# Kernel tuning notes

Hardware: AMD Instinct MI355X
Metric: run time of the kernel (lower is better)

The kernel has to match this reference:

```python
import jax, jax.numpy as jnp
import numpy as np
from jax.scipy.linalg import expm

B, T, N_IN, N_HID, N_OUT = 8192, 2048, 2, 10, 10


def setup_inputs() -> dict:
    key = jax.random.key(0)
    k0, k1, k2, k3, k4 = jax.random.split(key, 5)
    inputs = jax.random.normal(k0, (B, T, N_IN), dtype=jnp.float32)
    # skew-symmetric seed for the orthogonal recurrent kernel (expm parametrization)
    A = jax.random.normal(k1, (N_HID, N_HID), dtype=jnp.float32) * 0.1
    # input_kernel: nn.Linear(n_inputs, n_hidden, bias=False) -> weight [H, D_in]
    W_in = jax.random.normal(k2, (N_HID, N_IN), dtype=jnp.float32) / np.sqrt(N_IN)
    # modrelu bias, initialized uniform(-0.01, 0.01) as in exprnn
    b_mod = jax.random.uniform(k3, (N_HID,), jnp.float32, -0.01, 0.01)
    # final nn.Linear(n_hidden, n_outputs)
    lin_W = jax.random.normal(k4, (N_OUT, N_HID), dtype=jnp.float32) / np.sqrt(N_HID)
    lin_b = jnp.zeros((N_OUT,), jnp.float32)
    return {"inputs": inputs, "A": A, "W_in": W_in, "b_mod": b_mod,
            "lin_W": lin_W, "lin_b": lin_b}


def _modrelu(z, b):
    # modrelu(z) = sign(z) * relu(|z| + b)
    return jnp.sign(z) * jax.nn.relu(jnp.abs(z) + b)


def reference(inputs, A, W_in, b_mod, lin_W, lin_b):
    # Orthogonal recurrent matrix: Bmat = expm(skew(A)), skew from strict upper triangle
    A_tri = jnp.triu(A, k=1)
    Bmat = expm(A_tri - A_tri.T)  # [H, H], orthogonal
    # Precompute input projections for all timesteps: [B, T, H]
    x_proj = jnp.einsum('btd,hd->bth', inputs, W_in)
    h0 = jnp.zeros((inputs.shape[0], W_in.shape[0]), dtype=inputs.dtype)

    def step(h, x_t):
        h_new = _modrelu(x_t + h @ Bmat, b_mod)
        return h_new, None

    hT, _ = jax.lax.scan(step, h0, jnp.swapaxes(x_proj, 0, 1))  # scan over time
    out = hT @ lin_W.T + lin_b  # [B, n_outputs]
    return out
```

## Files before the change

kernel.cpp:

```cpp
#include <hip/hip_runtime.h>
#include <hip/hip_bf16.h>

#define H 10
#define T_LEN 2048
#define BATCH 8192

__global__ void expm_kernel(const float* __restrict__ A, float* __restrict__ Bout) {
    __shared__ double S[H][H];
    __shared__ double P[H][H];
    __shared__ double E[H][H];
    const int tid = threadIdx.x;
    const int i = tid / H, j = tid % H;
    if (tid < H * H) {
        double a = 0.0;
        if (i < j) a = (double)A[i * H + j];
        else if (i > j) a = -(double)A[j * H + i];
        a *= (1.0 / 256.0);
        S[i][j] = a;
        P[i][j] = a;
        E[i][j] = (i == j ? 1.0 : 0.0) + a;
    }
    __syncthreads();
    for (int k = 2; k <= 16; ++k) {
        double acc = 0.0;
        if (tid < H * H) {
            for (int m = 0; m < H; ++m) acc += P[i][m] * S[m][j];
            acc *= (1.0 / (double)k);
        }
        __syncthreads();
        if (tid < H * H) { P[i][j] = acc; E[i][j] += acc; }
        __syncthreads();
    }
    for (int r = 0; r < 8; ++r) {
        double acc = 0.0;
        if (tid < H * H) {
            for (int m = 0; m < H; ++m) acc += E[i][m] * E[m][j];
        }
        __syncthreads();
        if (tid < H * H) E[i][j] = acc;
        __syncthreads();
    }
    if (tid < H * H) Bout[i * H + j] = (float)E[i][j];
}


#define GBCAST(hbits, i) \
    __int_as_float(__builtin_amdgcn_ds_swizzle((hbits), ((i) << 5) | 0x10))

__global__ __launch_bounds__(256, 2)
void rnn_kernel(const float* __restrict__ x,
                const float* __restrict__ Bm_g,
                const float* __restrict__ Win,
                const float* __restrict__ bmod,
                const float* __restrict__ lW,
                const float* __restrict__ lb,
                float* __restrict__ out) {
    const int r  = threadIdx.x & 15;
    const int bb = blockIdx.x * 16 + (threadIdx.x >> 4);
    const int j  = (r < H) ? r : (H - 1);

    float Bcol[H];
#pragma unroll
    for (int i = 0; i < H; ++i) Bcol[i] = Bm_g[i * H + j];

    const float w0 = Win[j * 2 + 0];
    const float w1 = Win[j * 2 + 1];
    const float bm = bmod[j];
    float h = 0.0f;

    const float4* __restrict__ xp4 =
        (const float4*)(x + (size_t)bb * (T_LEN * 2));

    float4 buf0 = xp4[0], buf1 = xp4[1], buf2 = xp4[2], buf3 = xp4[3];

    for (int t0 = 0; t0 < T_LEN; t0 += 8) {
        const float4 c0 = buf0, c1 = buf1, c2 = buf2, c3 = buf3;
        if (t0 + 8 < T_LEN) {
            const int base = (t0 + 8) >> 1;
            buf0 = xp4[base + 0];
            buf1 = xp4[base + 1];
            buf2 = xp4[base + 2];
            buf3 = xp4[base + 3];
        }
        float xs[16];
        xs[0] = c0.x; xs[1] = c0.y; xs[2]  = c0.z; xs[3]  = c0.w;
        xs[4] = c1.x; xs[5] = c1.y; xs[6]  = c1.z; xs[7]  = c1.w;
        xs[8] = c2.x; xs[9] = c2.y; xs[10] = c2.z; xs[11] = c2.w;
        xs[12] = c3.x; xs[13] = c3.y; xs[14] = c3.z; xs[15] = c3.w;

#pragma unroll
        for (int u = 0; u < 8; ++u) {
            const float x0 = xs[2 * u], x1 = xs[2 * u + 1];
            float acc = fmaf(x1, w1, x0 * w0);
            const int hbits = __float_as_int(h);
            acc = fmaf(GBCAST(hbits, 0), Bcol[0], acc);
            acc = fmaf(GBCAST(hbits, 1), Bcol[1], acc);
            acc = fmaf(GBCAST(hbits, 2), Bcol[2], acc);
            acc = fmaf(GBCAST(hbits, 3), Bcol[3], acc);
            acc = fmaf(GBCAST(hbits, 4), Bcol[4], acc);
            acc = fmaf(GBCAST(hbits, 5), Bcol[5], acc);
            acc = fmaf(GBCAST(hbits, 6), Bcol[6], acc);
            acc = fmaf(GBCAST(hbits, 7), Bcol[7], acc);
            acc = fmaf(GBCAST(hbits, 8), Bcol[8], acc);
            acc = fmaf(GBCAST(hbits, 9), Bcol[9], acc);
            const float rr = fmaxf(fabsf(acc) + bm, 0.0f);
            h = __builtin_copysignf(rr, acc);
        }
    }

    const int hbits = __float_as_int(h);
    float hb[H];
    hb[0] = GBCAST(hbits, 0); hb[1] = GBCAST(hbits, 1);
    hb[2] = GBCAST(hbits, 2); hb[3] = GBCAST(hbits, 3);
    hb[4] = GBCAST(hbits, 4); hb[5] = GBCAST(hbits, 5);
    hb[6] = GBCAST(hbits, 6); hb[7] = GBCAST(hbits, 7);
    hb[8] = GBCAST(hbits, 8); hb[9] = GBCAST(hbits, 9);
    if (r < H) {
        float acc = lb[r];
#pragma unroll
        for (int jj = 0; jj < H; ++jj) acc = fmaf(hb[jj], lW[r * H + jj], acc);
        out[(size_t)bb * H + r] = acc;
    }
}

extern "C" void kernel_launch(void* const* d_in, const int* in_sizes, int n_in,
                              void* d_out, int out_size, void* d_ws, size_t ws_size,
                              hipStream_t stream) {
    const float* inputs = (const float*)d_in[0];
    const float* A      = (const float*)d_in[1];
    const float* W_in   = (const float*)d_in[2];
    const float* b_mod  = (const float*)d_in[3];
    const float* lin_W  = (const float*)d_in[4];
    const float* lin_b  = (const float*)d_in[5];
    float* out = (float*)d_out;
    float* Bmat = (float*)d_ws;

    expm_kernel<<<1, 128, 0, stream>>>(A, Bmat);
    rnn_kernel<<<BATCH / 16, 256, 0, stream>>>(inputs, Bmat, W_in, b_mod,
                                               lin_W, lin_b, out);
}
```

Baseline: 392.7 us.

## Pack six batch rows per wave and broadcast hidden state through LDS

The RNN kernel now maps 10 lanes to each batch row instead of 16, so one 64-thread block covers 6 rows and few lanes sit idle. The previous per-step ten ds_swizzle broadcasts of the hidden state are replaced by one LDS write, a barrier and three vector LDS reads. The matrix-vector product is split into two accumulators to shorten the dependent FMA chain. The aim is fewer total waves and fewer cross-lane operations per timestep. The cost is a barrier on every step of the serial recurrence and lower per-CU occupancy with single-wave blocks.

```diff
diff --git a/kernel.cpp b/kernel.cpp
--- a/kernel.cpp
+++ b/kernel.cpp
@@ -4,6 +4,7 @@
 #define H 10
 #define T_LEN 2048
 #define BATCH 8192
+#define GPW 6
 
 __global__ void expm_kernel(const float* __restrict__ A, float* __restrict__ Bout) {
     __shared__ double S[H][H];
@@ -31,7 +32,7 @@
         if (tid < H * H) { P[i][j] = acc; E[i][j] += acc; }
         __syncthreads();
     }
-    for (int r = 0; r < 8; ++r) {
+    for (int rr = 0; rr < 8; ++rr) {
         double acc = 0.0;
         if (tid < H * H) {
             for (int m = 0; m < H; ++m) acc += E[i][m] * E[m][j];
@@ -43,11 +44,7 @@
     if (tid < H * H) Bout[i * H + j] = (float)E[i][j];
 }
 
-
-#define GBCAST(hbits, i) \
-    __int_as_float(__builtin_amdgcn_ds_swizzle((hbits), ((i) << 5) | 0x10))
-
-__global__ __launch_bounds__(256, 2)
+__global__ __launch_bounds__(64)
 void rnn_kernel(const float* __restrict__ x,
                 const float* __restrict__ Bm_g,
                 const float* __restrict__ Win,
@@ -55,17 +52,22 @@
                 const float* __restrict__ lW,
                 const float* __restrict__ lb,
                 float* __restrict__ out) {
-    const int r  = threadIdx.x & 15;
-    const int bb = blockIdx.x * 16 + (threadIdx.x >> 4);
-    const int j  = (r < H) ? r : (H - 1);
+    __shared__ float hsh[(GPW + 1) * 12];
+
+    const int lane = threadIdx.x;
+    const int g = lane / 10;
+    const int r = lane - g * 10;
+    const int bb_raw = blockIdx.x * GPW + g;
+    const bool active = (g < GPW) && (bb_raw < BATCH);
+    const int bb = active ? bb_raw : 0;
+    float* const hb = &hsh[g * 12];
 
     float Bcol[H];
 #pragma unroll
-    for (int i = 0; i < H; ++i) Bcol[i] = Bm_g[i * H + j];
-
-    const float w0 = Win[j * 2 + 0];
-    const float w1 = Win[j * 2 + 1];
-    const float bm = bmod[j];
+    for (int i = 0; i < H; ++i) Bcol[i] = Bm_g[i * H + r];
+    const float w0 = Win[r * 2 + 0];
+    const float w1 = Win[r * 2 + 1];
+    const float bm = bmod[r];
     float h = 0.0f;
 
     const float4* __restrict__ xp4 =
@@ -91,34 +93,47 @@
 #pragma unroll
         for (int u = 0; u < 8; ++u) {
             const float x0 = xs[2 * u], x1 = xs[2 * u + 1];
+            hb[r] = h;
+            __syncthreads();
+            const float4 ha = *(const float4*)(hb);
+            const float4 hbv = *(const float4*)(hb + 4);
+            const float2 hc = *(const float2*)(hb + 8);
+
             float acc = fmaf(x1, w1, x0 * w0);
-            const int hbits = __float_as_int(h);
-            acc = fmaf(GBCAST(hbits, 0), Bcol[0], acc);
-            acc = fmaf(GBCAST(hbits, 1), Bcol[1], acc);
-            acc = fmaf(GBCAST(hbits, 2), Bcol[2], acc);
-            acc = fmaf(GBCAST(hbits, 3), Bcol[3], acc);
-            acc = fmaf(GBCAST(hbits, 4), Bcol[4], acc);
-            acc = fmaf(GBCAST(hbits, 5), Bcol[5], acc);
-            acc = fmaf(GBCAST(hbits, 6), Bcol[6], acc);
-            acc = fmaf(GBCAST(hbits, 7), Bcol[7], acc);
-            acc = fmaf(GBCAST(hbits, 8), Bcol[8], acc);
-            acc = fmaf(GBCAST(hbits, 9), Bcol[9], acc);
+            float cA = ha.x * Bcol[0];
+            float cB = ha.y * Bcol[1];
+            cA = fmaf(ha.z,  Bcol[2], cA);
+            cB = fmaf(ha.w,  Bcol[3], cB);
+            cA = fmaf(hbv.x, Bcol[4], cA);
+            cB = fmaf(hbv.y, Bcol[5], cB);
+            cA = fmaf(hbv.z, Bcol[6], cA);
+            cB = fmaf(hbv.w, Bcol[7], cB);
+            cA = fmaf(hc.x,  Bcol[8], cA);
+            cB = fmaf(hc.y,  Bcol[9], cB);
+            acc = acc + cA + cB;
+
             const float rr = fmaxf(fabsf(acc) + bm, 0.0f);
             h = __builtin_copysignf(rr, acc);
         }
     }
 
-    const int hbits = __float_as_int(h);
-    float hb[H];
-    hb[0] = GBCAST(hbits, 0); hb[1] = GBCAST(hbits, 1);
-    hb[2] = GBCAST(hbits, 2); hb[3] = GBCAST(hbits, 3);
-    hb[4] = GBCAST(hbits, 4); hb[5] = GBCAST(hbits, 5);
-    hb[6] = GBCAST(hbits, 6); hb[7] = GBCAST(hbits, 7);
-    hb[8] = GBCAST(hbits, 8); hb[9] = GBCAST(hbits, 9);
-    if (r < H) {
+    hb[r] = h;
+    __syncthreads();
+    const float4 ha = *(const float4*)(hb);
+    const float4 hbv = *(const float4*)(hb + 4);
+    const float2 hc = *(const float2*)(hb + 8);
+    if (active) {
         float acc = lb[r];
-#pragma unroll
-        for (int jj = 0; jj < H; ++jj) acc = fmaf(hb[jj], lW[r * H + jj], acc);
+        acc = fmaf(ha.x,  lW[r * H + 0], acc);
+        acc = fmaf(ha.y,  lW[r * H + 1], acc);
+        acc = fmaf(ha.z,  lW[r * H + 2], acc);
+        acc = fmaf(ha.w,  lW[r * H + 3], acc);
+        acc = fmaf(hbv.x, lW[r * H + 4], acc);
+        acc = fmaf(hbv.y, lW[r * H + 5], acc);
+        acc = fmaf(hbv.z, lW[r * H + 6], acc);
+        acc = fmaf(hbv.w, lW[r * H + 7], acc);
+        acc = fmaf(hc.x,  lW[r * H + 8], acc);
+        acc = fmaf(hc.y,  lW[r * H + 9], acc);
         out[(size_t)bb * H + r] = acc;
     }
 }
@@ -136,6 +151,7 @@
     float* Bmat = (float*)d_ws;
 
     expm_kernel<<<1, 128, 0, stream>>>(A, Bmat);
-    rnn_kernel<<<BATCH / 16, 256, 0, stream>>>(inputs, Bmat, W_in, b_mod,
-                                               lin_W, lin_b, out);
+    const int nblocks = (BATCH + GPW - 1) / GPW;
+    rnn_kernel<<<nblocks, 64, 0, stream>>>(inputs, Bmat, W_in, b_mod,
+                                           lin_W, lin_b, out);
 }
```

After: 360.8 us. 1.09x faster.

## Replace ds_swizzle broadcasts with DPP row shifts and split FMA chains

Applied to the files above, without the earlier changes.

The per-step hidden-state exchange now uses DPP row_shr/row_shl shifts instead of ds_swizzle broadcasts, with the recurrent matrix zero-padded to 16x16 so that out-of-row lanes contribute zero. The single serial chain of 10 FMAs becomes four independent accumulators summed at the end, which shortens the dependency chain on the recurrence's critical path. DPP modifiers fold into the VALU op and avoid the LDS-unit latency of swizzle. The cost is more FMAs per step (19 shifts instead of 10 broadcasts) and a small shared-memory epilogue for the final linear layer.

```diff
diff --git a/kernel.cpp b/kernel.cpp
--- a/kernel.cpp
+++ b/kernel.cpp
@@ -2,6 +2,7 @@
 #include <hip/hip_bf16.h>
 
 #define H 10
+#define HP 16
 #define T_LEN 2048
 #define BATCH 8192
 
@@ -31,7 +32,7 @@
         if (tid < H * H) { P[i][j] = acc; E[i][j] += acc; }
         __syncthreads();
     }
-    for (int r = 0; r < 8; ++r) {
+    for (int rr = 0; rr < 8; ++rr) {
         double acc = 0.0;
         if (tid < H * H) {
             for (int m = 0; m < H; ++m) acc += E[i][m] * E[m][j];
@@ -40,32 +41,42 @@
         if (tid < H * H) E[i][j] = acc;
         __syncthreads();
     }
-    if (tid < H * H) Bout[i * H + j] = (float)E[i][j];
+    for (int idx = tid; idx < HP * HP; idx += blockDim.x) {
+        const int i2 = idx / HP, j2 = idx % HP;
+        Bout[idx] = (i2 < H && j2 < H) ? (float)E[i2][j2] : 0.0f;
+    }
 }
 
 
-#define GBCAST(hbits, i) \
-    __int_as_float(__builtin_amdgcn_ds_swizzle((hbits), ((i) << 5) | 0x10))
+#define DPP_SHR(vbits, k) \
+    __int_as_float(__builtin_amdgcn_update_dpp(0, (vbits), 0x110 + (k), 0xF, 0xF, true))
+#define DPP_SHL(vbits, k) \
+    __int_as_float(__builtin_amdgcn_update_dpp(0, (vbits), 0x100 + (k), 0xF, 0xF, true))
 
 __global__ __launch_bounds__(256, 2)
 void rnn_kernel(const float* __restrict__ x,
-                const float* __restrict__ Bm_g,
+                const float* __restrict__ Bp,
                 const float* __restrict__ Win,
                 const float* __restrict__ bmod,
                 const float* __restrict__ lW,
                 const float* __restrict__ lb,
                 float* __restrict__ out) {
-    const int r  = threadIdx.x & 15;
-    const int bb = blockIdx.x * 16 + (threadIdx.x >> 4);
-    const int j  = (r < H) ? r : (H - 1);
+    const int tid = threadIdx.x;
+    const int r = tid & 15;
+    const int g = tid >> 4;
+    const int bb = blockIdx.x * 16 + g;
 
-    float Bcol[H];
+    const float Bown = Bp[r * HP + r];
+    float BvS[10], BvL[10];
 #pragma unroll
-    for (int i = 0; i < H; ++i) Bcol[i] = Bm_g[i * H + j];
-
-    const float w0 = Win[j * 2 + 0];
-    const float w1 = Win[j * 2 + 1];
-    const float bm = bmod[j];
+    for (int k = 1; k <= 9; ++k) {
+        BvS[k] = Bp[((r - k) & 15) * HP + r];
+        BvL[k] = Bp[((r + k) & 15) * HP + r];
+    }
+    const bool live = (r < H);
+    const float w0 = live ? Win[r * 2 + 0] : 0.0f;
+    const float w1 = live ? Win[r * 2 + 1] : 0.0f;
+    const float bm = live ? bmod[r] : 0.0f;
     float h = 0.0f;
 
     const float4* __restrict__ xp4 =
@@ -91,34 +102,44 @@
 #pragma unroll
         for (int u = 0; u < 8; ++u) {
             const float x0 = xs[2 * u], x1 = xs[2 * u + 1];
-            float acc = fmaf(x1, w1, x0 * w0);
             const int hbits = __float_as_int(h);
-            acc = fmaf(GBCAST(hbits, 0), Bcol[0], acc);
-            acc = fmaf(GBCAST(hbits, 1), Bcol[1], acc);
-            acc = fmaf(GBCAST(hbits, 2), Bcol[2], acc);
-            acc = fmaf(GBCAST(hbits, 3), Bcol[3], acc);
-            acc = fmaf(GBCAST(hbits, 4), Bcol[4], acc);
-            acc = fmaf(GBCAST(hbits, 5), Bcol[5], acc);
-            acc = fmaf(GBCAST(hbits, 6), Bcol[6], acc);
-            acc = fmaf(GBCAST(hbits, 7), Bcol[7], acc);
-            acc = fmaf(GBCAST(hbits, 8), Bcol[8], acc);
-            acc = fmaf(GBCAST(hbits, 9), Bcol[9], acc);
-            const float rr = fmaxf(fabsf(acc) + bm, 0.0f);
-            h = __builtin_copysignf(rr, acc);
+            float cA = x0 * w0;
+            float cB = x1 * w1;
+            float cC = h * Bown;
+            float cD = DPP_SHR(hbits, 1) * BvS[1];
+            cA = fmaf(DPP_SHR(hbits, 2), BvS[2], cA);
+            cB = fmaf(DPP_SHR(hbits, 3), BvS[3], cB);
+            cC = fmaf(DPP_SHR(hbits, 4), BvS[4], cC);
+            cD = fmaf(DPP_SHR(hbits, 5), BvS[5], cD);
+            cA = fmaf(DPP_SHR(hbits, 6), BvS[6], cA);
+            cB = fmaf(DPP_SHR(hbits, 7), BvS[7], cB);
+            cC = fmaf(DPP_SHR(hbits, 8), BvS[8], cC);
+            cD = fmaf(DPP_SHR(hbits, 9), BvS[9], cD);
+            cA = fmaf(DPP_SHL(hbits, 1), BvL[1], cA);
+            cB = fmaf(DPP_SHL(hbits, 2), BvL[2], cB);
+            cC = fmaf(DPP_SHL(hbits, 3), BvL[3], cC);
+            cD = fmaf(DPP_SHL(hbits, 4), BvL[4], cD);
+            cA = fmaf(DPP_SHL(hbits, 5), BvL[5], cA);
+            cB = fmaf(DPP_SHL(hbits, 6), BvL[6], cB);
+            cC = fmaf(DPP_SHL(hbits, 7), BvL[7], cC);
+            cD = fmaf(DPP_SHL(hbits, 8), BvL[8], cD);
+            cA = fmaf(DPP_SHL(hbits, 9), BvL[9], cA);
+            const float acc = (cA + cB) + (cC + cD);
+
+            const float az = fabsf(acc) + bm;
+            const float rr2 = fmaxf(az, 0.0f);
+            h = __builtin_copysignf(rr2, acc);
         }
     }
 
-    const int hbits = __float_as_int(h);
-    float hb[H];
-    hb[0] = GBCAST(hbits, 0); hb[1] = GBCAST(hbits, 1);
-    hb[2] = GBCAST(hbits, 2); hb[3] = GBCAST(hbits, 3);
-    hb[4] = GBCAST(hbits, 4); hb[5] = GBCAST(hbits, 5);
-    hb[6] = GBCAST(hbits, 6); hb[7] = GBCAST(hbits, 7);
-    hb[8] = GBCAST(hbits, 8); hb[9] = GBCAST(hbits, 9);
-    if (r < H) {
+    __shared__ float hsh[16][17];
+    hsh[g][r] = h;
+    __syncthreads();
+    if (live) {
         float acc = lb[r];
 #pragma unroll
-        for (int jj = 0; jj < H; ++jj) acc = fmaf(hb[jj], lW[r * H + jj], acc);
+        for (int jj = 0; jj < H; ++jj)
+            acc = fmaf(hsh[g][jj], lW[r * H + jj], acc);
         out[(size_t)bb * H + r] = acc;
     }
 }
@@ -133,9 +154,9 @@
     const float* lin_W  = (const float*)d_in[4];
     const float* lin_b  = (const float*)d_in[5];
     float* out = (float*)d_out;
-    float* Bmat = (float*)d_ws;
+    float* Bpad = (float*)d_ws;
 
-    expm_kernel<<<1, 128, 0, stream>>>(A, Bmat);
-    rnn_kernel<<<BATCH / 16, 256, 0, stream>>>(inputs, Bmat, W_in, b_mod,
+    expm_kernel<<<1, 128, 0, stream>>>(A, Bpad);
+    rnn_kernel<<<BATCH / 16, 256, 0, stream>>>(inputs, Bpad, W_in, b_mod,
                                                lin_W, lin_b, out);
 }
```

After: 465.8 us. 18.6% more time.
